# Performance work log

Hardware: AMD Instinct MI355X
Metric: run time of the kernel (lower is better)

## Reference

```python
import jax, jax.numpy as jnp
import numpy as np

L, C, F, H, W = 4, 512, 2048, 8, 4   # layers, channels, filter, heads, window
HD = C // H                          # head_dim = 64
B, T = 4, 1024
EPS = 1e-6


def setup_inputs() -> dict:
    key = jax.random.key(0)
    ks = jax.random.split(key, 12)
    def n(k, shape, s=0.02):
        return jax.random.normal(k, shape, dtype=jnp.float32) * s
    return {
        "x": jax.random.normal(ks[0], (B, C, T), dtype=jnp.float32),
        "mask": jnp.ones((B, 1, T), dtype=jnp.float32),
        "qw": n(ks[1], (L, C, C)), "qb": jnp.zeros((L, C), jnp.float32),
        "kw": n(ks[2], (L, C, C)), "kb": jnp.zeros((L, C), jnp.float32),
        "vw": n(ks[3], (L, C, C)), "vb": jnp.zeros((L, C), jnp.float32),
        "ow": n(ks[4], (L, C, C)), "ob": jnp.zeros((L, C), jnp.float32),
        "emb_rel_k": n(ks[5], (L, 2 * W + 1, HD), 0.01),
        "emb_rel_v": n(ks[6], (L, 2 * W + 1, HD), 0.01),
        "ln1_g": jnp.ones((L, C), jnp.float32), "ln1_b": jnp.zeros((L, C), jnp.float32),
        "w1": n(ks[7], (L, F, C)), "b1": jnp.zeros((L, F), jnp.float32),
        "w2": n(ks[8], (L, C, F)), "b2": jnp.zeros((L, C), jnp.float32),
        "ln2_g": jnp.ones((L, C), jnp.float32), "ln2_b": jnp.zeros((L, C), jnp.float32),
    }


def _conv1(x, w, b):
    # 1x1 Conv1d: (B,Cin,T) x (Cout,Cin) -> (B,Cout,T)
    return jnp.einsum('oc,bct->bot', w, x) + b[None, :, None]


def _ln(x, g, b):
    # LayerNorm over channel dim of (B,C,T)
    m = jnp.mean(x, axis=1, keepdims=True)
    v = jnp.var(x, axis=1, keepdims=True)
    return (x - m) * jax.lax.rsqrt(v + EPS) * g[None, :, None] + b[None, :, None]


def reference(x, mask, qw, qb, kw, kb, vw, vb, ow, ob, emb_rel_k, emb_rel_v,
              ln1_g, ln1_b, w1, b1, w2, b2, ln2_g, ln2_b):
    Bv, Cv, Tv = x.shape
    pos = jnp.arange(Tv)
    rel = pos[None, :] - pos[:, None]           # (T,T) j - i
    outside = jnp.abs(rel) > W
    idx = jnp.clip(rel, -W, W) + W              # (T,T) in [0, 2W]
    am = mask[:, :, None, :]                    # (B,1,1,T)
    inv_scale = 1.0 / jnp.sqrt(jnp.float32(HD))
    for i in range(L):
        res = x
        q = _conv1(x, qw[i], qb[i]).reshape(Bv, H, HD, Tv).transpose(0, 1, 3, 2) * inv_scale
        k = _conv1(x, kw[i], kb[i]).reshape(Bv, H, HD, Tv).transpose(0, 1, 3, 2)
        v = _conv1(x, vw[i], vb[i]).reshape(Bv, H, HD, Tv).transpose(0, 1, 3, 2)
        rk = jnp.where(outside[:, :, None], 0.0, emb_rel_k[i][idx])  # (T,T,HD)
        rv = jnp.where(outside[:, :, None], 0.0, emb_rel_v[i][idx])
        scores = jnp.einsum('bhid,bhjd->bhij', q, k) + jnp.einsum('bhid,ijd->bhij', q, rk)
        scores = jnp.where(am == 0, -jnp.inf, scores)
        attn = jax.nn.softmax(scores, axis=-1)
        o = jnp.einsum('bhij,bhjd->bhid', attn, v) + jnp.einsum('bhij,ijd->bhid', attn, rv)
        o = o.transpose(0, 1, 3, 2).reshape(Bv, Cv, Tv)
        x = _ln(res + _conv1(o, ow[i], ob[i]), ln1_g[i], ln1_b[i])
        res = x
        h = jax.nn.relu(_conv1(x * mask, w1[i], b1[i])) * mask
        h = _conv1(h, w2[i], b2[i]) * mask
        x = _ln(res + h, ln2_g[i], ln2_b[i])
        x = x * mask
    return x
```

## Files before the change

### kernel.cpp

```cpp
#include <hip/hip_runtime.h>

#define BQ 4
#define CQ 512
#define TQ 1024
#define FQ 2048
#define LQ 4
#define HQ 8
#define MT (BQ * TQ)

typedef __attribute__((ext_vector_type(8))) short short8;
typedef __attribute__((ext_vector_type(4))) float floatx4;

#define MFMA16(a, b, c) __builtin_amdgcn_mfma_f32_16x16x32_bf16(a, b, c, 0, 0, 0)

static __device__ __forceinline__ unsigned short f2bf(float f) {
  union { float f; unsigned u; } v; v.f = f;
  unsigned r = v.u + 0x7fff + ((v.u >> 16) & 1);
  return (unsigned short)(r >> 16);
}

static __device__ __forceinline__ void async_copy16(const void* g, void* l) {
  __builtin_amdgcn_global_load_lds(
      (const __attribute__((address_space(1))) void*)g,
      (__attribute__((address_space(3))) void*)l, 16, 0, 0);
}

__global__ __launch_bounds__(256) void mfma_gemm(
    const unsigned short* __restrict__ A, const unsigned short* __restrict__ B,
    void* __restrict__ Y, const float* __restrict__ bias,
    const float* __restrict__ mask, int M, int N, int K, int lda, int ldb,
    long long kofs, long long sYb, float scale, int flags)
{
  const int tid = threadIdx.x;
  const int w = tid >> 6, lane = tid & 63;
  const int wm = w >> 1, wn = w & 1;
  const int m0 = blockIdx.y * 128, n0 = blockIdx.x * 128;
  const size_t ko = (size_t)blockIdx.z * kofs;

  __shared__ unsigned short sA[128 * 64];
  __shared__ unsigned short sB[128 * 64];

  floatx4 acc[4][4];
#pragma unroll
  for (int i = 0; i < 4; i++)
#pragma unroll
    for (int j = 0; j < 4; j++) acc[i][j] = floatx4{0.f, 0.f, 0.f, 0.f};

  const int col = lane & 15, gq = lane >> 4;
  const int xsw = col & 7;

  for (int k0 = 0; k0 < K; k0 += 64) {
#pragma unroll
    for (int r = 0; r < 4; r++) {
      const int cbase = w * 64 + r * 256;
      const int c = cbase + lane;
      const int row = c >> 3, p = c & 7;
      const int gb = (p ^ (row & 7)) * 8;
      async_copy16(&A[(size_t)(m0 + row) * lda + ko + k0 + gb], &sA[cbase * 8]);
      async_copy16(&B[(size_t)(n0 + row) * ldb + ko + k0 + gb], &sB[cbase * 8]);
    }
    __syncthreads();
#pragma unroll
    for (int kh = 0; kh < 2; kh++) {
      const int q = kh * 4 + gq;
      const int so = (q ^ xsw) * 8;
      short8 af[4], bfr[4];
#pragma unroll
      for (int im = 0; im < 4; im++)
        af[im] = *(const short8*)&sA[(wm * 64 + im * 16 + col) * 64 + so];
#pragma unroll
      for (int in = 0; in < 4; in++)
        bfr[in] = *(const short8*)&sB[(wn * 64 + in * 16 + col) * 64 + so];
#pragma unroll
      for (int im = 0; im < 4; im++)
#pragma unroll
        for (int in = 0; in < 4; in++)
          acc[im][in] = MFMA16(af[im], bfr[in], acc[im][in]);
    }
    __syncthreads();
  }

  const bool relu  = flags & 1;
  const bool prem  = flags & 2;
  const bool postm = flags & 4;
  const bool bf16o = flags & 16;
  const bool raw   = flags & 32;
  float* Yf = (float*)Y + (size_t)blockIdx.z * sYb;
  unsigned short* Yh = (unsigned short*)Y;

#pragma unroll
  for (int im = 0; im < 4; im++)
#pragma unroll
    for (int in = 0; in < 4; in++) {
      int nn = n0 + wn * 64 + in * 16 + col;
      float bn = raw ? 0.f : bias[nn];
#pragma unroll
      for (int reg = 0; reg < 4; reg++) {
        int mm = m0 + wm * 64 + im * 16 + gq * 4 + reg;
        float val = acc[im][in][reg];
        if (raw) {
          Yf[(size_t)mm * N + nn] = val;
        } else {
          float mv = (prem || postm) ? mask[mm] : 1.f;
          if (prem) val *= mv;
          val = (val + bn) * scale;
          if (relu) val = fmaxf(val, 0.f);
          if (postm) val *= mv;
          if (bf16o) Yh[(size_t)mm * N + nn] = f2bf(val);
          else       Yf[(size_t)mm * N + nn] = val;
        }
      }
    }
}

__global__ __launch_bounds__(256) void mfma_gemm64(
    const unsigned short* __restrict__ A, const unsigned short* __restrict__ B,
    float* __restrict__ Y, int M, int N, int K, int lda, int ldb,
    long long kofs, long long sYb)
{
  const int tid = threadIdx.x;
  const int w = tid >> 6, lane = tid & 63;
  const int wm = w >> 1, wn = w & 1;
  const int m0 = blockIdx.y * 128, n0 = blockIdx.x * 64;
  const size_t ko = (size_t)blockIdx.z * kofs;

  __shared__ unsigned short sA[128 * 64];
  __shared__ unsigned short sB[64 * 64];

  floatx4 acc[4][2];
#pragma unroll
  for (int i = 0; i < 4; i++)
#pragma unroll
    for (int j = 0; j < 2; j++) acc[i][j] = floatx4{0.f, 0.f, 0.f, 0.f};

  const int col = lane & 15, gq = lane >> 4;
  const int xsw = col & 7;

  for (int k0 = 0; k0 < K; k0 += 64) {
#pragma unroll
    for (int r = 0; r < 4; r++) {
      const int cbase = w * 64 + r * 256;
      const int c = cbase + lane;
      const int row = c >> 3, p = c & 7;
      const int gb = (p ^ (row & 7)) * 8;
      async_copy16(&A[(size_t)(m0 + row) * lda + ko + k0 + gb], &sA[cbase * 8]);
    }
#pragma unroll
    for (int r = 0; r < 2; r++) {
      const int cbase = w * 64 + r * 256;
      const int c = cbase + lane;
      const int row = c >> 3, p = c & 7;
      const int gb = (p ^ (row & 7)) * 8;
      async_copy16(&B[(size_t)(n0 + row) * ldb + ko + k0 + gb], &sB[cbase * 8]);
    }
    __syncthreads();
#pragma unroll
    for (int kh = 0; kh < 2; kh++) {
      const int q = kh * 4 + gq;
      const int so = (q ^ xsw) * 8;
      short8 af[4], bfr[2];
#pragma unroll
      for (int im = 0; im < 4; im++)
        af[im] = *(const short8*)&sA[(wm * 64 + im * 16 + col) * 64 + so];
#pragma unroll
      for (int in = 0; in < 2; in++)
        bfr[in] = *(const short8*)&sB[(wn * 32 + in * 16 + col) * 64 + so];
#pragma unroll
      for (int im = 0; im < 4; im++)
#pragma unroll
        for (int in = 0; in < 2; in++)
          acc[im][in] = MFMA16(af[im], bfr[in], acc[im][in]);
    }
    __syncthreads();
  }

  float* Yf = Y + (size_t)blockIdx.z * sYb;
#pragma unroll
  for (int im = 0; im < 4; im++)
#pragma unroll
    for (int in = 0; in < 2; in++) {
      int nn = n0 + wn * 32 + in * 16 + col;
#pragma unroll
      for (int reg = 0; reg < 4; reg++) {
        int mm = m0 + wm * 64 + im * 16 + gq * 4 + reg;
        Yf[(size_t)mm * N + nn] = acc[im][in][reg];
      }
    }
}

__global__ __launch_bounds__(256) void qkv_gemm(
    const unsigned short* __restrict__ A, const unsigned short* __restrict__ B,
    unsigned short* __restrict__ qo, unsigned short* __restrict__ ko2,
    unsigned short* __restrict__ vo, const float* __restrict__ qb,
    const float* __restrict__ kb, const float* __restrict__ vb)
{
  const int tid = threadIdx.x;
  const int w = tid >> 6, lane = tid & 63;
  const int wm = w >> 1, wn = w & 1;
  const int m0 = blockIdx.y * 128, n0 = blockIdx.x * 128;

  __shared__ unsigned short sA[128 * 64];
  __shared__ unsigned short sB[128 * 64];

  floatx4 acc[4][4];
#pragma unroll
  for (int i = 0; i < 4; i++)
#pragma unroll
    for (int j = 0; j < 4; j++) acc[i][j] = floatx4{0.f, 0.f, 0.f, 0.f};

  const int col = lane & 15, gq = lane >> 4;
  const int xsw = col & 7;

  for (int k0 = 0; k0 < CQ; k0 += 64) {
#pragma unroll
    for (int r = 0; r < 4; r++) {
      const int cbase = w * 64 + r * 256;
      const int c = cbase + lane;
      const int row = c >> 3, p = c & 7;
      const int gb = (p ^ (row & 7)) * 8;
      async_copy16(&A[(size_t)(m0 + row) * CQ + k0 + gb], &sA[cbase * 8]);
      async_copy16(&B[(size_t)(n0 + row) * CQ + k0 + gb], &sB[cbase * 8]);
    }
    __syncthreads();
#pragma unroll
    for (int kh = 0; kh < 2; kh++) {
      const int q = kh * 4 + gq;
      const int so = (q ^ xsw) * 8;
      short8 af[4], bfr[4];
#pragma unroll
      for (int im = 0; im < 4; im++)
        af[im] = *(const short8*)&sA[(wm * 64 + im * 16 + col) * 64 + so];
#pragma unroll
      for (int in = 0; in < 4; in++)
        bfr[in] = *(const short8*)&sB[(wn * 64 + in * 16 + col) * 64 + so];
#pragma unroll
      for (int im = 0; im < 4; im++)
#pragma unroll
        for (int in = 0; in < 4; in++)
          acc[im][in] = MFMA16(af[im], bfr[in], acc[im][in]);
    }
    __syncthreads();
  }

  const int seg = n0 >> 9;
  const int nbase = n0 - seg * 512;

  if (seg < 2) {
    unsigned short* Yh = (seg == 0) ? qo : ko2;
    const float* bp = (seg == 0) ? qb : kb;
    const float scale = (seg == 0) ? 0.125f : 1.f;
#pragma unroll
    for (int im = 0; im < 4; im++)
#pragma unroll
      for (int in = 0; in < 4; in++) {
        int nn = nbase + wn * 64 + in * 16 + col;
        float bn = bp[nn];
#pragma unroll
        for (int reg = 0; reg < 4; reg++) {
          int mm = m0 + wm * 64 + im * 16 + gq * 4 + reg;
          Yh[(size_t)mm * CQ + nn] = f2bf((acc[im][in][reg] + bn) * scale);
        }
      }
  } else {
#pragma unroll
    for (int im = 0; im < 4; im++)
#pragma unroll
      for (int in = 0; in < 4; in++) {
        int nn = nbase + wn * 64 + in * 16 + col;
        float bn = vb[nn];
        int mm0 = m0 + wm * 64 + im * 16 + gq * 4;
        int bz = mm0 >> 10, t = mm0 & 1023;
        ushort4 uv = {f2bf(acc[im][in][0] + bn), f2bf(acc[im][in][1] + bn),
                      f2bf(acc[im][in][2] + bn), f2bf(acc[im][in][3] + bn)};
        *(ushort4*)&vo[((size_t)bz * CQ + nn) * TQ + t] = uv;
      }
  }
}

__global__ __launch_bounds__(256) void attn_kernel(
    const unsigned short* __restrict__ qt, const unsigned short* __restrict__ kt,
    const unsigned short* __restrict__ vt, const float* __restrict__ mask,
    const float* __restrict__ rk, const float* __restrict__ rv,
    unsigned short* __restrict__ o)
{
  const int b = blockIdx.z, h = blockIdx.y;
  const int w = threadIdx.x >> 6;
  const int lane = threadIdx.x & 63;
  const int col = lane & 15, g = lane >> 4;
  const int i0 = blockIdx.x * 64 + w * 16;

  const unsigned short* qb = qt + (size_t)b * TQ * CQ + h * 64;
  const unsigned short* kb = kt + (size_t)b * TQ * CQ + h * 64;
  const unsigned short* vb = vt + ((size_t)b * CQ + h * 64) * TQ;
  unsigned short* ob = o + (size_t)b * TQ * CQ + h * 64;

  __shared__ unsigned short sK[2][64 * 64];
  __shared__ unsigned short sV[2][64 * 64];
  __shared__ unsigned short pbuf[4][16][72];
  __shared__ float rkdl[4][16][9];
  __shared__ float pband[4][16][9];
  __shared__ float smask[TQ];

  short8 qf0 = *(const short8*)&qb[(size_t)(i0 + col) * CQ + g * 8];
  short8 qf1 = *(const short8*)&qb[(size_t)(i0 + col) * CQ + 32 + g * 8];

  {
    short8 rb0 = {0, 0, 0, 0, 0, 0, 0, 0}, rb1 = rb0;
    if (col < 9) {
#pragma unroll
      for (int i = 0; i < 8; i++) {
        rb0[i] = (short)f2bf(rk[col * 64 + g * 8 + i]);
        rb1[i] = (short)f2bf(rk[col * 64 + 32 + g * 8 + i]);
      }
    }
    floatx4 rc = {0.f, 0.f, 0.f, 0.f};
    rc = MFMA16(qf0, rb0, rc);
    rc = MFMA16(qf1, rb1, rc);
    if (col < 9) {
#pragma unroll
      for (int reg = 0; reg < 4; reg++) rkdl[w][g * 4 + reg][col] = rc[reg];
    }
  }
  for (int e = lane; e < 144; e += 64) pband[w][e / 9][e % 9] = 0.f;
  {
    float4 mvv = *(const float4*)&mask[(size_t)b * TQ + threadIdx.x * 4];
    *(float4*)&smask[threadIdx.x * 4] = mvv;
  }

  const int prow = lane >> 3;
  const int pblk = (lane & 7) ^ prow;
  const int eblk0 = ((0 * 4 + g) ^ (col & 7)) * 8;
  const int eblk1 = ((1 * 4 + g) ^ (col & 7)) * 8;

#pragma unroll
  for (int q = 0; q < 2; q++) {
    int s = w * 2 + q;
    async_copy16(&kb[(size_t)(s * 8 + prow) * CQ + pblk * 8], &sK[0][s * 512]);
    async_copy16(&vb[(size_t)(s * 8 + prow) * TQ + 0 + pblk * 8], &sV[0][s * 512]);
  }

  float l_lane[4] = {0.f, 0.f, 0.f, 0.f};
  floatx4 oacc[4];
#pragma unroll
  for (int r = 0; r < 4; r++) oacc[r] = floatx4{0.f, 0.f, 0.f, 0.f};

  for (int jt = 0; jt < 16; jt++) {
    const int cur = jt & 1, nx = cur ^ 1;
    __syncthreads();
    if (jt < 15) {
      const int j0n = (jt + 1) * 64;
#pragma unroll
      for (int q = 0; q < 2; q++) {
        int s = w * 2 + q;
        async_copy16(&kb[(size_t)(j0n + s * 8 + prow) * CQ + pblk * 8],
                     &sK[nx][s * 512]);
        async_copy16(&vb[(size_t)(s * 8 + prow) * TQ + j0n + pblk * 8],
                     &sV[nx][s * 512]);
      }
    }
    const int j0 = jt * 64;

    floatx4 sc[4];
#pragma unroll
    for (int jg = 0; jg < 4; jg++) {
      const int r = (jg * 16 + col) * 64;
      short8 kf0 = *(const short8*)&sK[cur][r + eblk0];
      short8 kf1 = *(const short8*)&sK[cur][r + eblk1];
      floatx4 z = {0.f, 0.f, 0.f, 0.f};
      z = MFMA16(qf0, kf0, z);
      sc[jg] = MFMA16(qf1, kf1, z);
    }

    const bool inband = (j0 <= i0 + 19) && (j0 + 63 >= i0 - 4);

    float p[4][4];
#pragma unroll
    for (int reg = 0; reg < 4; reg++) {
      const int ig = i0 + g * 4 + reg;
#pragma unroll
      for (int jg = 0; jg < 4; jg++) {
        float s = sc[jg][reg];
        if (inband) {
          int dlt = j0 + jg * 16 + col - ig + 4;
          if (dlt >= 0 && dlt < 9) s += rkdl[w][g * 4 + reg][dlt];
        }
        float pv = (smask[j0 + jg * 16 + col] == 0.f) ? 0.f : __expf(s);
        p[reg][jg] = pv;
        l_lane[reg] += pv;
      }
    }

    if (inband) {
#pragma unroll
      for (int reg = 0; reg < 4; reg++) {
        const int row = g * 4 + reg;
#pragma unroll
        for (int jg = 0; jg < 4; jg++) {
          int dlt = j0 + jg * 16 + col - (i0 + row) + 4;
          if (dlt >= 0 && dlt < 9) pband[w][row][dlt] = p[reg][jg];
        }
      }
    }

#pragma unroll
    for (int reg = 0; reg < 4; reg++)
#pragma unroll
      for (int jg = 0; jg < 4; jg++)
        pbuf[w][g * 4 + reg][jg * 16 + col] = f2bf(p[reg][jg]);
    __builtin_amdgcn_wave_barrier();
    short8 pf0 = *(const short8*)&pbuf[w][col][g * 8];
    short8 pf1 = *(const short8*)&pbuf[w][col][32 + g * 8];

#pragma unroll
    for (int dg = 0; dg < 4; dg++) {
      const int r = (dg * 16 + col) * 64;
      short8 vf0 = *(const short8*)&sV[cur][r + eblk0];
      short8 vf1 = *(const short8*)&sV[cur][r + eblk1];
      oacc[dg] = MFMA16(pf0, vf0, oacc[dg]);
      oacc[dg] = MFMA16(pf1, vf1, oacc[dg]);
    }
    __builtin_amdgcn_wave_barrier();
  }

  float inv_l[4];
#pragma unroll
  for (int reg = 0; reg < 4; reg++) {
    float l = l_lane[reg];
#pragma unroll
    for (int off = 1; off < 16; off <<= 1) l += __shfl_xor(l, off, 64);
    inv_l[reg] = 1.f / l;
  }

#pragma unroll
  for (int dg = 0; dg < 4; dg++) {
    float rvc[4] = {0.f, 0.f, 0.f, 0.f};
#pragma unroll
    for (int dlt = 0; dlt < 9; dlt++) {
      float rvv = rv[dlt * 64 + dg * 16 + col];
#pragma unroll
      for (int reg = 0; reg < 4; reg++)
        rvc[reg] += pband[w][g * 4 + reg][dlt] * rvv;
    }
#pragma unroll
    for (int reg = 0; reg < 4; reg++) {
      float val = (oacc[dg][reg] + rvc[reg]) * inv_l[reg];
      ob[(size_t)(i0 + g * 4 + reg) * CQ + dg * 16 + col] = f2bf(val);
    }
  }
}

__global__ __launch_bounds__(256) void ln_rows(
    const float* __restrict__ res, const float* __restrict__ a1,
    const float* __restrict__ a2, const float* __restrict__ addb,
    const float* __restrict__ g, const float* __restrict__ bb,
    const float* __restrict__ mask, float* __restrict__ outf,
    unsigned short* __restrict__ outb, int mode)
{
  const int row = blockIdx.x * 4 + (threadIdx.x >> 6);
  const int lane = threadIdx.x & 63;
  const size_t base = (size_t)row * CQ + lane * 8;
  const int c0 = lane * 8;

  float mv = mask[row];
  float sadd = (mode & 1) ? mv : 1.f;

  float v[8];
#pragma unroll
  for (int i = 0; i < 8; i += 4) {
    float4 r = *(const float4*)&res[base + i];
    float4 x1 = *(const float4*)&a1[base + i];
    float4 x2 = *(const float4*)&a2[base + i];
    float4 bv = *(const float4*)&addb[c0 + i];
    v[i + 0] = r.x + sadd * (x1.x + x2.x + bv.x);
    v[i + 1] = r.y + sadd * (x1.y + x2.y + bv.y);
    v[i + 2] = r.z + sadd * (x1.z + x2.z + bv.z);
    v[i + 3] = r.w + sadd * (x1.w + x2.w + bv.w);
  }
  float sum = 0.f, ssq = 0.f;
#pragma unroll
  for (int i = 0; i < 8; i++) { sum += v[i]; ssq += v[i] * v[i]; }
#pragma unroll
  for (int off = 1; off < 64; off <<= 1) {
    sum += __shfl_xor(sum, off, 64);
    ssq += __shfl_xor(ssq, off, 64);
  }
  float mean = sum * (1.f / CQ);
  float var = ssq * (1.f / CQ) - mean * mean;
  float rstd = rsqrtf(var + 1e-6f);
  float pm = (mode & 2) ? mv : 1.f;

  float y[8];
#pragma unroll
  for (int i = 0; i < 8; i++)
    y[i] = ((v[i] - mean) * rstd * g[c0 + i] + bb[c0 + i]) * pm;
  float4 o0 = {y[0], y[1], y[2], y[3]}, o1 = {y[4], y[5], y[6], y[7]};
  *(float4*)&outf[base] = o0;
  *(float4*)&outf[base + 4] = o1;
  if (outb) {
    ushort4 u0 = {f2bf(y[0]), f2bf(y[1]), f2bf(y[2]), f2bf(y[3])};
    ushort4 u1 = {f2bf(y[4]), f2bf(y[5]), f2bf(y[6]), f2bf(y[7])};
    *(ushort4*)&outb[base] = u0;
    *(ushort4*)&outb[base + 4] = u1;
  }
}

__global__ __launch_bounds__(256) void tr_in(
    const float* __restrict__ x, float* __restrict__ xa,
    unsigned short* __restrict__ xab)
{
  __shared__ float s[32][33];
  const int b = blockIdx.z, t0 = blockIdx.x * 32, c0 = blockIdx.y * 32;
  const int tx = threadIdx.x, ty = threadIdx.y;
#pragma unroll
  for (int r = 0; r < 4; r++)
    s[ty + r * 8][tx] = x[((size_t)b * CQ + c0 + ty + r * 8) * TQ + t0 + tx];
  __syncthreads();
#pragma unroll
  for (int r = 0; r < 4; r++) {
    float v = s[tx][ty + r * 8];
    size_t idx = ((size_t)b * TQ + t0 + ty + r * 8) * CQ + c0 + tx;
    xa[idx] = v;
    xab[idx] = f2bf(v);
  }
}

__global__ __launch_bounds__(256) void tr_out(
    const float* __restrict__ y, float* __restrict__ out)
{
  __shared__ float s[32][33];
  const int b = blockIdx.z, t0 = blockIdx.x * 32, c0 = blockIdx.y * 32;
  const int tx = threadIdx.x, ty = threadIdx.y;
#pragma unroll
  for (int r = 0; r < 4; r++)
    s[ty + r * 8][tx] = y[((size_t)b * TQ + t0 + ty + r * 8) * CQ + c0 + tx];
  __syncthreads();
#pragma unroll
  for (int r = 0; r < 4; r++)
    out[((size_t)b * CQ + c0 + ty + r * 8) * TQ + t0 + tx] = s[tx][ty + r * 8];
}

__global__ __launch_bounds__(256) void wconv_all(
    const float* __restrict__ qw, const float* __restrict__ kw,
    const float* __restrict__ vw, const float* __restrict__ ow,
    const float* __restrict__ w1, const float* __restrict__ w2,
    unsigned short* __restrict__ dst)
{
  const int PER_L4 = 786432;
  int idx4 = blockIdx.x * 256 + threadIdx.x;
  int l = idx4 / PER_L4;
  int e = (idx4 - l * PER_L4) * 4;
  const float* src;
  size_t off;
  if (e < 786432) {
    int which = e >> 18;
    src = (which == 0) ? qw : (which == 1) ? kw : vw;
    off = (size_t)l * 262144 + (e & 262143);
  } else if (e < 1048576) {
    src = ow;  off = (size_t)l * 262144 + (e - 786432);
  } else if (e < 2097152) {
    src = w1;  off = (size_t)l * 1048576 + (e - 1048576);
  } else {
    src = w2;  off = (size_t)l * 1048576 + (e - 2097152);
  }
  float4 v = *(const float4*)&src[off];
  ushort4 u = {f2bf(v.x), f2bf(v.y), f2bf(v.z), f2bf(v.w)};
  *(ushort4*)&dst[(size_t)l * 3145728 + e] = u;
}

extern "C" void kernel_launch(void* const* d_in, const int* in_sizes, int n_in,
                              void* d_out, int out_size, void* d_ws, size_t ws_size,
                              hipStream_t stream) {
  const float* x    = (const float*)d_in[0];
  const float* mask = (const float*)d_in[1];
  const float* qw   = (const float*)d_in[2];
  const float* qbb  = (const float*)d_in[3];
  const float* kw   = (const float*)d_in[4];
  const float* kbb  = (const float*)d_in[5];
  const float* vw   = (const float*)d_in[6];
  const float* vbb  = (const float*)d_in[7];
  const float* ow   = (const float*)d_in[8];
  const float* obb  = (const float*)d_in[9];
  const float* rk   = (const float*)d_in[10];
  const float* rv   = (const float*)d_in[11];
  const float* g1   = (const float*)d_in[12];
  const float* be1  = (const float*)d_in[13];
  const float* w1   = (const float*)d_in[14];
  const float* b1   = (const float*)d_in[15];
  const float* w2   = (const float*)d_in[16];
  const float* b2   = (const float*)d_in[17];
  const float* g2   = (const float*)d_in[18];
  const float* be2  = (const float*)d_in[19];
  float* out = (float*)d_out;

  const size_t MB = 1 << 20;
  char* base = (char*)d_ws;
  unsigned short* wbufA = (unsigned short*)(base);
  float*          xa    = (float*)(base + 24 * MB);
  unsigned short* xab   = (unsigned short*)(base + 32 * MB);
  unsigned short* qtb   = (unsigned short*)(base + 36 * MB);
  unsigned short* ktb   = (unsigned short*)(base + 40 * MB);
  unsigned short* vtb   = (unsigned short*)(base + 44 * MB);
  unsigned short* obufb = (unsigned short*)(base + 48 * MB);
  float*          t1    = (float*)(base + 52 * MB);
  unsigned short* hbuf  = qtb;

  const long long sY = (long long)MT * CQ;
  float* t1b = t1 + sY;

  dim3 b256(256);
  dim3 gtr(TQ / 32, CQ / 32, BQ);
  dim3 gln(MT / 4);

  hipLaunchKernelGGL(tr_in, gtr, dim3(32, 8), 0, stream, x, xa, xab);
  hipLaunchKernelGGL(wconv_all, dim3(12288), b256, 0, stream,
      qw, kw, vw, ow, w1, w2, wbufA);

  for (int i = 0; i < LQ; i++) {
    const unsigned short* wl  = wbufA + (size_t)i * 3145728;
    const unsigned short* wo  = wl + 786432;
    const unsigned short* wf1 = wl + 1048576;
    const unsigned short* wf2 = wl + 2097152;
    hipLaunchKernelGGL(qkv_gemm, dim3(12, 32), b256, 0, stream,
        xab, wl, qtb, ktb, vtb, qbb + i * CQ, kbb + i * CQ, vbb + i * CQ);
    hipLaunchKernelGGL(attn_kernel, dim3(TQ / 64, HQ, BQ), b256, 0, stream,
        qtb, ktb, vtb, mask, rk + (size_t)i * 576, rv + (size_t)i * 576, obufb);
    hipLaunchKernelGGL(mfma_gemm64, dim3(8, 32, 2), b256, 0, stream,
        obufb, wo, t1, MT, CQ, CQ / 2, CQ, CQ, (long long)(CQ / 2), sY);
    hipLaunchKernelGGL(ln_rows, gln, b256, 0, stream,
        xa, t1, t1b, obb + i * CQ, g1 + i * CQ, be1 + i * CQ, mask,
        xa, xab, 0);
    hipLaunchKernelGGL(mfma_gemm, dim3(16, 32, 1), b256, 0, stream,
        xab, wf1, (void*)hbuf, b1 + i * FQ, mask,
        MT, FQ, CQ, CQ, CQ, 0LL, 0LL, 1.f, 1 | 2 | 4 | 16);
    hipLaunchKernelGGL(mfma_gemm64, dim3(8, 32, 2), b256, 0, stream,
        hbuf, wf2, t1, MT, CQ, FQ / 2, FQ, FQ, (long long)(FQ / 2), sY);
    hipLaunchKernelGGL(ln_rows, gln, b256, 0, stream,
        xa, t1, t1b, b2 + i * CQ, g2 + i * CQ, be2 + i * CQ, mask,
        xa, xab, 3);
  }
  hipLaunchKernelGGL(tr_out, gtr, dim3(32, 8), 0, stream, xa, out);
}
```

Before: 634.0 us.

## Double-buffer LDS tiles in GEMM kernels to overlap loads with MFMA

```diff
diff --git a/kernel.cpp b/kernel.cpp
--- a/kernel.cpp
+++ b/kernel.cpp
@@ -37,8 +37,8 @@
   const int m0 = blockIdx.y * 128, n0 = blockIdx.x * 128;
   const size_t ko = (size_t)blockIdx.z * kofs;
 
-  __shared__ unsigned short sA[128 * 64];
-  __shared__ unsigned short sB[128 * 64];
+  __shared__ unsigned short sA[2][128 * 64];
+  __shared__ unsigned short sB[2][128 * 64];
 
   floatx4 acc[4][4];
 #pragma unroll
@@ -49,17 +49,26 @@
   const int col = lane & 15, gq = lane >> 4;
   const int xsw = col & 7;
 
-  for (int k0 = 0; k0 < K; k0 += 64) {
+  auto stage = [&](int buf, int k0) {
 #pragma unroll
     for (int r = 0; r < 4; r++) {
       const int cbase = w * 64 + r * 256;
       const int c = cbase + lane;
       const int row = c >> 3, p = c & 7;
       const int gb = (p ^ (row & 7)) * 8;
-      async_copy16(&A[(size_t)(m0 + row) * lda + ko + k0 + gb], &sA[cbase * 8]);
-      async_copy16(&B[(size_t)(n0 + row) * ldb + ko + k0 + gb], &sB[cbase * 8]);
-    }
+      async_copy16(&A[(size_t)(m0 + row) * lda + ko + k0 + gb],
+                   &sA[buf][cbase * 8]);
+      async_copy16(&B[(size_t)(n0 + row) * ldb + ko + k0 + gb],
+                   &sB[buf][cbase * 8]);
+    }
+  };
+
+  stage(0, 0);
+  const int nit = K >> 6;
+  for (int it = 0; it < nit; it++) {
+    const int cur = it & 1;
     __syncthreads();
+    if (it + 1 < nit) stage(cur ^ 1, (it + 1) << 6);
 #pragma unroll
     for (int kh = 0; kh < 2; kh++) {
       const int q = kh * 4 + gq;
@@ -67,17 +76,16 @@
       short8 af[4], bfr[4];
 #pragma unroll
       for (int im = 0; im < 4; im++)
-        af[im] = *(const short8*)&sA[(wm * 64 + im * 16 + col) * 64 + so];
+        af[im] = *(const short8*)&sA[cur][(wm * 64 + im * 16 + col) * 64 + so];
 #pragma unroll
       for (int in = 0; in < 4; in++)
-        bfr[in] = *(const short8*)&sB[(wn * 64 + in * 16 + col) * 64 + so];
+        bfr[in] = *(const short8*)&sB[cur][(wn * 64 + in * 16 + col) * 64 + so];
 #pragma unroll
       for (int im = 0; im < 4; im++)
 #pragma unroll
         for (int in = 0; in < 4; in++)
           acc[im][in] = MFMA16(af[im], bfr[in], acc[im][in]);
     }
-    __syncthreads();
   }
 
   const bool relu  = flags & 1;
@@ -124,8 +132,8 @@
   const int m0 = blockIdx.y * 128, n0 = blockIdx.x * 64;
   const size_t ko = (size_t)blockIdx.z * kofs;
 
-  __shared__ unsigned short sA[128 * 64];
-  __shared__ unsigned short sB[64 * 64];
+  __shared__ unsigned short sA[2][128 * 64];
+  __shared__ unsigned short sB[2][64 * 64];
 
   floatx4 acc[4][2];
 #pragma unroll
@@ -136,14 +144,15 @@
   const int col = lane & 15, gq = lane >> 4;
   const int xsw = col & 7;
 
-  for (int k0 = 0; k0 < K; k0 += 64) {
+  auto stage = [&](int buf, int k0) {
 #pragma unroll
     for (int r = 0; r < 4; r++) {
       const int cbase = w * 64 + r * 256;
       const int c = cbase + lane;
       const int row = c >> 3, p = c & 7;
       const int gb = (p ^ (row & 7)) * 8;
-      async_copy16(&A[(size_t)(m0 + row) * lda + ko + k0 + gb], &sA[cbase * 8]);
+      async_copy16(&A[(size_t)(m0 + row) * lda + ko + k0 + gb],
+                   &sA[buf][cbase * 8]);
     }
 #pragma unroll
     for (int r = 0; r < 2; r++) {
@@ -151,9 +160,17 @@
       const int c = cbase + lane;
       const int row = c >> 3, p = c & 7;
       const int gb = (p ^ (row & 7)) * 8;
-      async_copy16(&B[(size_t)(n0 + row) * ldb + ko + k0 + gb], &sB[cbase * 8]);
-    }
+      async_copy16(&B[(size_t)(n0 + row) * ldb + ko + k0 + gb],
+                   &sB[buf][cbase * 8]);
+    }
+  };
+
+  stage(0, 0);
+  const int nit = K >> 6;
+  for (int it = 0; it < nit; it++) {
+    const int cur = it & 1;
     __syncthreads();
+    if (it + 1 < nit) stage(cur ^ 1, (it + 1) << 6);
 #pragma unroll
     for (int kh = 0; kh < 2; kh++) {
       const int q = kh * 4 + gq;
@@ -161,17 +178,16 @@
       short8 af[4], bfr[2];
 #pragma unroll
       for (int im = 0; im < 4; im++)
-        af[im] = *(const short8*)&sA[(wm * 64 + im * 16 + col) * 64 + so];
+        af[im] = *(const short8*)&sA[cur][(wm * 64 + im * 16 + col) * 64 + so];
 #pragma unroll
       for (int in = 0; in < 2; in++)
-        bfr[in] = *(const short8*)&sB[(wn * 32 + in * 16 + col) * 64 + so];
+        bfr[in] = *(const short8*)&sB[cur][(wn * 32 + in * 16 + col) * 64 + so];
 #pragma unroll
       for (int im = 0; im < 4; im++)
 #pragma unroll
         for (int in = 0; in < 2; in++)
           acc[im][in] = MFMA16(af[im], bfr[in], acc[im][in]);
     }
-    __syncthreads();
   }
 
   float* Yf = Y + (size_t)blockIdx.z * sYb;
@@ -199,8 +215,8 @@
   const int wm = w >> 1, wn = w & 1;
   const int m0 = blockIdx.y * 128, n0 = blockIdx.x * 128;
 
-  __shared__ unsigned short sA[128 * 64];
-  __shared__ unsigned short sB[128 * 64];
+  __shared__ unsigned short sA[2][128 * 64];
+  __shared__ unsigned short sB[2][128 * 64];
 
   floatx4 acc[4][4];
 #pragma unroll
@@ -211,17 +227,24 @@
   const int col = lane & 15, gq = lane >> 4;
   const int xsw = col & 7;
 
-  for (int k0 = 0; k0 < CQ; k0 += 64) {
+  auto stage = [&](int buf, int k0) {
 #pragma unroll
     for (int r = 0; r < 4; r++) {
       const int cbase = w * 64 + r * 256;
       const int c = cbase + lane;
       const int row = c >> 3, p = c & 7;
       const int gb = (p ^ (row & 7)) * 8;
-      async_copy16(&A[(size_t)(m0 + row) * CQ + k0 + gb], &sA[cbase * 8]);
-      async_copy16(&B[(size_t)(n0 + row) * CQ + k0 + gb], &sB[cbase * 8]);
-    }
+      async_copy16(&A[(size_t)(m0 + row) * CQ + k0 + gb], &sA[buf][cbase * 8]);
+      async_copy16(&B[(size_t)(n0 + row) * CQ + k0 + gb], &sB[buf][cbase * 8]);
+    }
+  };
+
+  stage(0, 0);
+  const int nit = CQ >> 6;
+  for (int it = 0; it < nit; it++) {
+    const int cur = it & 1;
     __syncthreads();
+    if (it + 1 < nit) stage(cur ^ 1, (it + 1) << 6);
 #pragma unroll
     for (int kh = 0; kh < 2; kh++) {
       const int q = kh * 4 + gq;
@@ -229,17 +252,16 @@
       short8 af[4], bfr[4];
 #pragma unroll
       for (int im = 0; im < 4; im++)
-        af[im] = *(const short8*)&sA[(wm * 64 + im * 16 + col) * 64 + so];
+        af[im] = *(const short8*)&sA[cur][(wm * 64 + im * 16 + col) * 64 + so];
 #pragma unroll
       for (int in = 0; in < 4; in++)
-        bfr[in] = *(const short8*)&sB[(wn * 64 + in * 16 + col) * 64 + so];
+        bfr[in] = *(const short8*)&sB[cur][(wn * 64 + in * 16 + col) * 64 + so];
 #pragma unroll
       for (int im = 0; im < 4; im++)
 #pragma unroll
         for (int in = 0; in < 4; in++)
           acc[im][in] = MFMA16(af[im], bfr[in], acc[im][in]);
     }
-    __syncthreads();
   }
 
   const int seg = n0 >> 9;
```

After: 626.3 us. No clear change (-1.2%).
